# Kernel tuning notes

Hardware: AMD Instinct MI355X
Metric: run time of the kernel (lower is better)

The kernel has to match this reference:

```python
import jax, jax.numpy as jnp
import numpy as np

N_NODES = 50000
N_EDGES = 800000
HID = 64
N_GRAPHS = 64


def setup_inputs() -> dict:
    key = jax.random.key(0)
    ks = jax.random.split(key, 12)
    x = jax.random.normal(ks[0], (N_NODES, 1), dtype=jnp.float32)
    edge_index = jax.random.randint(ks[1], (2, N_EDGES), 0, N_NODES, dtype=jnp.int64)
    batch = jnp.sort(jax.random.randint(ks[2], (N_NODES,), 0, N_GRAPHS, dtype=jnp.int64))
    def glorot(k, shape):
        fan_in, fan_out = shape
        s = jnp.sqrt(2.0 / (fan_in + fan_out)).astype(jnp.float32)
        return jax.random.normal(k, shape, dtype=jnp.float32) * s
    return {
        "x": x, "edge_index": edge_index, "batch": batch,
        "W1l": glorot(ks[3], (1, HID)), "b1": jnp.zeros((HID,), jnp.float32), "W1r": glorot(ks[4], (1, HID)),
        "W2l": glorot(ks[5], (HID, HID)), "b2": jnp.zeros((HID,), jnp.float32), "W2r": glorot(ks[6], (HID, HID)),
        "W3l": glorot(ks[7], (HID, HID)), "b3": jnp.zeros((HID,), jnp.float32), "W3r": glorot(ks[8], (HID, HID)),
        "Wfc1": glorot(ks[9], (HID, HID // 2)), "bfc1": jnp.zeros((HID // 2,), jnp.float32),
        "Wfc2": glorot(ks[10], (HID // 2, 1)), "bfc2": jnp.zeros((1,), jnp.float32),
    }


def _sage_conv(x, src, dst, Wl, bl, Wr):
    # PyG SAGEConv (mean aggr): lin_l(mean_{j in N(i)} x_j) + lin_r(x_i)
    msgs = x[src]                                                   # [E, d] gather
    agg = jax.ops.segment_sum(msgs, dst, num_segments=N_NODES)      # [N, d] scatter-add
    cnt = jax.ops.segment_sum(jnp.ones((src.shape[0], 1), x.dtype), dst, num_segments=N_NODES)
    mean = agg / jnp.maximum(cnt, 1.0)                              # isolated nodes -> 0
    return mean @ Wl + bl + x @ Wr


def reference(x, edge_index, batch,
              W1l, b1, W1r, W2l, b2, W2r, W3l, b3, W3r,
              Wfc1, bfc1, Wfc2, bfc2):
    src, dst = edge_index[0], edge_index[1]
    layers = [(W1l, b1, W1r), (W2l, b2, W2r), (W3l, b3, W3r)]
    h = x
    for (Wl, bl, Wr) in layers:
        h_res = h
        h = jax.nn.relu(_sage_conv(h, src, dst, Wl, bl, Wr))
        # dropout is identity at inference; residual broadcasts [N,64]+[N,1] on layer 1
        h = h + h_res
    # global mean pool over graphs in the batch
    sums = jax.ops.segment_sum(h, batch, num_segments=N_GRAPHS)     # [G, d]
    cnts = jax.ops.segment_sum(jnp.ones((h.shape[0], 1), h.dtype), batch, num_segments=N_GRAPHS)
    pooled = sums / jnp.maximum(cnts, 1.0)
    out = jax.nn.relu(pooled @ Wfc1 + bfc1)
    out = out @ Wfc2 + bfc2                                          # [G, 1]
    return out
```

## Files before the change

kernel.cpp:

```cpp
#include <hip/hip_runtime.h>
#include <hip/hip_bf16.h>
#include <hip/hip_fp16.h>

#define HID 64
#define NGRAPHS 64
#define BUCKET 64
#define CAP 4096
#define EPB 2048
#define NSLOT 33

typedef _Float16 half8 __attribute__((ext_vector_type(8)));
typedef float floatx4 __attribute__((ext_vector_type(4)));

__global__ __launch_bounds__(256) void detect_init_kernel(const void* edge, const void* batch,
                                                          int* flags, int* bcursor,
                                                          float* psum,
                                                          const float* W2l, const float* W2r,
                                                          const float* W3l, const float* W3r,
                                                          __half* wl2h, __half* wr2h,
                                                          __half* wl3h, __half* wr3h,
                                                          int E2, int N, int G, int NB) {
    int t = threadIdx.x;
    for (int i = t; i < NB; i += 256) bcursor[i] = i * CAP;
    for (int i = t; i < G * HID; i += 256) psum[i] = 0.0f;
    for (int i = t; i < HID * HID; i += 256) {
        wl2h[i] = __float2half(W2l[i]);
        wr2h[i] = __float2half(W2r[i]);
        wl3h[i] = __float2half(W3l[i]);
        wr3h[i] = __float2half(W3r[i]);
    }
    if (t < 64) {
        int lane = t;
        int half_ = E2 / 2;
        int stride = half_ / 64; if (stride < 1) stride = 1;
        int j = lane * stride; if (j >= half_) j = half_ - 1;
        long long v = ((const long long*)edge)[j];
        bool ok = (v >= 0 && v < (long long)N);
        unsigned long long m = __ballot(ok);
        if (lane == 0) flags[0] = (m == ~0ULL) ? 1 : 0;
        int halfB = N / 2;
        int strideB = halfB / 64; if (strideB < 1) strideB = 1;
        int jb = lane * strideB; if (jb >= halfB) jb = halfB - 1;
        long long vb = ((const long long*)batch)[jb];
        bool okb = (vb >= 0 && vb < (long long)G);
        unsigned long long mb = __ballot(okb);
        if (lane == 0) flags[1] = (mb == ~0ULL) ? 1 : 0;
    }
}

__device__ __forceinline__ int idx_at(const void* p, int i, bool is64) {
    return is64 ? (int)((const long long*)p)[i] : ((const int*)p)[i];
}

__global__ __launch_bounds__(256) void bin_scatter_kernel(const void* edge, const int* __restrict__ flags,
                                                          int* __restrict__ bcursor,
                                                          unsigned int* __restrict__ entries,
                                                          int E, int NB) {
    extern __shared__ int lds[];
    int* hist = lds;
    int* base = lds + NB;
    int* ssrc = lds + 2 * NB;
    int* sdst = ssrc + EPB;
    for (int i = threadIdx.x; i < NB; i += 256) hist[i] = 0;
    __syncthreads();
    bool is64 = flags[0] != 0;
    int start = blockIdx.x * EPB;
    int end = start + EPB; if (end > E) end = E;
    int cnt = end - start;
    for (int k = threadIdx.x; k < cnt; k += 256) {
        int e = start + k;
        int srcv = idx_at(edge, e, is64);
        int d = idx_at(edge, E + e, is64);
        ssrc[k] = srcv;
        sdst[k] = d;
        atomicAdd(&hist[d >> 6], 1);
    }
    __syncthreads();
    for (int i = threadIdx.x; i < NB; i += 256) {
        int h = hist[i];
        base[i] = h ? atomicAdd(&bcursor[i], h) : 0;
    }
    __syncthreads();
    for (int i = threadIdx.x; i < NB; i += 256) hist[i] = 0;
    __syncthreads();
    for (int k = threadIdx.x; k < cnt; k += 256) {
        int d = sdst[k];
        int b = d >> 6;
        int lo = atomicAdd(&hist[b], 1);
        int p = base[b] + lo;
        if (p < (b + 1) * CAP)
            entries[p] = ((unsigned int)ssrc[k] << 6) | (unsigned int)(d & 63);
    }
}

__global__ __launch_bounds__(256) void csr_l1_kernel(const unsigned int* __restrict__ entries,
                                                     const int* __restrict__ bcursor,
                                                     const float* __restrict__ x,
                                                     const float* __restrict__ W1l,
                                                     const float* __restrict__ b1,
                                                     const float* __restrict__ W1r,
                                                     int* __restrict__ rowptr,
                                                     int* __restrict__ deg,
                                                     int* __restrict__ csr,
                                                     __half* __restrict__ h1h,
                                                     int N, int NB) {
    __shared__ int hist[BUCKET];
    __shared__ int lstart[BUCKET];
    __shared__ int lcur[BUCKET];
    __shared__ float accx[BUCKET];
    __shared__ float sx[BUCKET];
    int t = threadIdx.x;
    int b = blockIdx.x;
    int r0 = b * CAP;
    int cnt = bcursor[b] - r0; if (cnt > CAP) cnt = CAP;
    if (t < BUCKET) {
        hist[t] = 0; lcur[t] = 0; accx[t] = 0.0f;
        int node = b * BUCKET + t;
        sx[t] = (node < N) ? x[node] : 0.0f;
    }
    __syncthreads();
    for (int j = r0 + t; j < r0 + cnt; j += 256) {
        unsigned int en = entries[j];
        atomicAdd(&hist[en & 63u], 1);
        atomicAdd(&accx[en & 63u], x[en >> 6]);
    }
    __syncthreads();
    if (t < BUCKET) {
        int v = hist[t];
        int s = v;
#pragma unroll
        for (int off = 1; off < 64; off <<= 1) {
            int u = __shfl_up(s, off);
            if (t >= off) s += u;
        }
        lstart[t] = s - v;
        int node = b * BUCKET + t;
        if (node < N) {
            rowptr[node] = r0 + s - v;
            deg[node] = v;
        }
    }
    __syncthreads();
    for (int j = r0 + t; j < r0 + cnt; j += 256) {
        unsigned int en = entries[j];
        int dl = (int)(en & 63u);
        int p = atomicAdd(&lcur[dl], 1);
        csr[r0 + lstart[dl] + p] = (int)(en >> 6);
    }
    __syncthreads();
    int f = t & 63;
    int sub = t >> 6;
    float wlf = W1l[f], bf = b1[f], wrf = W1r[f];
    for (int it = 0; it < 16; ++it) {
        int nl = it * 4 + sub;
        int node = b * BUCKET + nl;
        if (node < N) {
            int d = hist[nl];
            float mv = (d > 0) ? accx[nl] / (float)d : 0.0f;
            float xv = sx[nl];
            float v = fmaf(mv, wlf, fmaf(xv, wrf, bf));
            v = v > 0.0f ? v : 0.0f;
            h1h[(size_t)node * HID + f] = __float2half(v + xv);
        }
    }
}

__global__ __launch_bounds__(256) void gather_mfma_kernel(const int* __restrict__ rowptr,
                                                          const int* __restrict__ deg,
                                                          const int* __restrict__ csr,
                                                          const __half* __restrict__ hph,
                                                          const __half* __restrict__ Wlh,
                                                          const float* __restrict__ bvec,
                                                          const __half* __restrict__ Wrh,
                                                          __half* __restrict__ houth,
                                                          float* __restrict__ psum,
                                                          const void* batch,
                                                          const int* __restrict__ flags,
                                                          int N) {
    __shared__ _Float16 smean[32][HID + 8];
    __shared__ float spool[NSLOT][HID];
    __shared__ int sb[32];
    int t = threadIdx.x;
    bool pool = (psum != nullptr);
    if (pool) {
        for (int i = t; i < NSLOT * HID; i += 256) ((float*)spool)[i] = 0.0f;
        if (t < 32) {
            int node = blockIdx.x * 32 + t;
            sb[t] = (node < N) ? idx_at(batch, node, flags[1] != 0) : -1;
        }
    }

    {
        int grp = t >> 3;
        int l = t & 7;
        int i = blockIdx.x * 32 + grp;
        if (i < N) {
            int r0 = rowptr[i];
            int d = deg[i];
            int r1 = r0 + d;
            float a[4][8];
#pragma unroll
            for (int w = 0; w < 4; ++w)
#pragma unroll
                for (int k = 0; k < 8; ++k) a[w][k] = 0.0f;
            int j = r0;
            for (; j + 8 <= r1; j += 8) {
                uint4 u[8];
#pragma unroll
                for (int m = 0; m < 8; ++m) {
                    int s = csr[j + m];
                    u[m] = *(const uint4*)(hph + (size_t)s * HID + l * 8);
                }
#pragma unroll
                for (int m = 0; m < 8; ++m) {
                    const __half2* p = (const __half2*)&u[m];
#pragma unroll
                    for (int q = 0; q < 4; ++q) {
                        float2 f2 = __half22float2(p[q]);
                        a[m & 3][2 * q]     += f2.x;
                        a[m & 3][2 * q + 1] += f2.y;
                    }
                }
            }
            for (; j + 4 <= r1; j += 4) {
                uint4 u[4];
#pragma unroll
                for (int m = 0; m < 4; ++m) {
                    int s = csr[j + m];
                    u[m] = *(const uint4*)(hph + (size_t)s * HID + l * 8);
                }
#pragma unroll
                for (int m = 0; m < 4; ++m) {
                    const __half2* p = (const __half2*)&u[m];
#pragma unroll
                    for (int q = 0; q < 4; ++q) {
                        float2 f2 = __half22float2(p[q]);
                        a[m][2 * q]     += f2.x;
                        a[m][2 * q + 1] += f2.y;
                    }
                }
            }
            for (; j < r1; ++j) {
                int s = csr[j];
                uint4 u0 = *(const uint4*)(hph + (size_t)s * HID + l * 8);
                const __half2* p = (const __half2*)&u0;
#pragma unroll
                for (int q = 0; q < 4; ++q) {
                    float2 f2 = __half22float2(p[q]);
                    a[0][2 * q]     += f2.x;
                    a[0][2 * q + 1] += f2.y;
                }
            }
            float inv = (d > 0) ? 1.0f / (float)d : 0.0f;
            __half2 o[4];
#pragma unroll
            for (int q = 0; q < 4; ++q) {
                float lo = ((a[0][2*q]   + a[1][2*q])   + (a[2][2*q]   + a[3][2*q]))   * inv;
                float hi = ((a[0][2*q+1] + a[1][2*q+1]) + (a[2][2*q+1] + a[3][2*q+1])) * inv;
                o[q] = __floats2half2_rn(lo, hi);
            }
            *(uint4*)&smean[grp][l * 8] = *(uint4*)o;
        }
    }
    __syncthreads();

    int wave = t >> 6;
    int lane = t & 63;
    int m = lane & 15;
    int quad = lane >> 4;
    int node0 = blockIdx.x * 32 + wave * 16;
    if (wave < 2 && node0 < N) {
        const _Float16* wlp = (const _Float16*)Wlh;
        const _Float16* wrp = (const _Float16*)Wrh;
        half8 bl[2][4], br[2][4];
#pragma unroll
        for (int kh = 0; kh < 2; ++kh)
#pragma unroll
            for (int nt = 0; nt < 4; ++nt) {
                half8 vl, vr;
#pragma unroll
                for (int j = 0; j < 8; ++j) {
                    int k = kh * 32 + quad * 8 + j;
                    vl[j] = wlp[k * HID + nt * 16 + m];
                    vr[j] = wrp[k * HID + nt * 16 + m];
                }
                bl[kh][nt] = vl;
                br[kh][nt] = vr;
            }
        int nlA = wave * 16 + m;
        half8 am0 = *(const half8*)&smean[nlA][quad * 8];
        half8 am1 = *(const half8*)&smean[nlA][32 + quad * 8];
        int nodeA = node0 + m; if (nodeA >= N) nodeA = N - 1;
        const _Float16* hrow = (const _Float16*)hph + (size_t)nodeA * HID;
        half8 ah0 = *(const half8*)(hrow + quad * 8);
        half8 ah1 = *(const half8*)(hrow + 32 + quad * 8);

#pragma unroll
        for (int nt = 0; nt < 4; ++nt) {
            float b = bvec[nt * 16 + m];
            floatx4 c = {b, b, b, b};
            c = __builtin_amdgcn_mfma_f32_16x16x32_f16(am0, bl[0][nt], c, 0, 0, 0);
            c = __builtin_amdgcn_mfma_f32_16x16x32_f16(am1, bl[1][nt], c, 0, 0, 0);
            c = __builtin_amdgcn_mfma_f32_16x16x32_f16(ah0, br[0][nt], c, 0, 0, 0);
            c = __builtin_amdgcn_mfma_f32_16x16x32_f16(ah1, br[1][nt], c, 0, 0, 0);
            int f = nt * 16 + m;
#pragma unroll
            for (int r = 0; r < 4; ++r) {
                int nodeR = node0 + quad * 4 + r;
                if (nodeR < N) {
                    float v = c[r];
                    v = v > 0.0f ? v : 0.0f;
                    v += __half2float(((const __half*)hph)[(size_t)nodeR * HID + f]);
                    if (!pool) {
                        houth[(size_t)nodeR * HID + f] = __float2half(v);
                    } else {
                        int bg = sb[wave * 16 + quad * 4 + r];
                        int slot = bg - sb[0];
                        if (slot < NSLOT) atomicAdd(&spool[slot][f], v);
                        else atomicAdd(&psum[bg * HID + f], v);
                    }
                }
            }
        }
    }

    if (pool) {
        __syncthreads();
        int gbase = sb[0];
        for (int i = t; i < NSLOT * HID; i += 256) {
            int s = i >> 6, f = i & 63;
            float v = spool[s][f];
            if (v != 0.0f) atomicAdd(&psum[(gbase + s) * HID + f], v);
        }
    }
}

__device__ __forceinline__ int lbound(const void* batch, int n, long long key, bool is64) {
    int lo = 0, hi = n;
    while (lo < hi) {
        int mid = (lo + hi) >> 1;
        long long v = is64 ? ((const long long*)batch)[mid] : (long long)((const int*)batch)[mid];
        if (v < key) lo = mid + 1; else hi = mid;
    }
    return lo;
}

__global__ __launch_bounds__(64) void fc_kernel(const float* __restrict__ psum,
                                                const void* batch,
                                                const int* __restrict__ flags,
                                                const float* __restrict__ Wfc1,
                                                const float* __restrict__ bfc1,
                                                const float* __restrict__ Wfc2,
                                                const float* __restrict__ bfc2,
                                                float* __restrict__ out, int N) {
    __shared__ int sb2[2];
    __shared__ float mean[HID];
    int g = blockIdx.x;
    int t = threadIdx.x;
    bool is64 = flags[1] != 0;
    if (t == 0) sb2[0] = lbound(batch, N, g, is64);
    if (t == 1) sb2[1] = lbound(batch, N, g + 1, is64);
    __syncthreads();
    float c = fmaxf((float)(sb2[1] - sb2[0]), 1.0f);
    mean[t] = psum[g * HID + t] / c;
    __syncthreads();
    float v = 0.0f;
    if (t < 32) {
        float acc = bfc1[t];
#pragma unroll
        for (int k = 0; k < HID; ++k) acc += mean[k] * Wfc1[k * 32 + t];
        float hcc = acc > 0.0f ? acc : 0.0f;
        v = hcc * Wfc2[t];
    }
#pragma unroll
    for (int off = 32; off >= 1; off >>= 1) v += __shfl_down(v, off);
    if (t == 0) out[g] = v + bfc2[0];
}

extern "C" void kernel_launch(void* const* d_in, const int* in_sizes, int n_in,
                              void* d_out, int out_size, void* d_ws, size_t ws_size,
                              hipStream_t stream) {
    const int N = in_sizes[0];
    const int E2 = in_sizes[1];
    const int E = E2 / 2;
    const int NB = (N + BUCKET - 1) / BUCKET;

    const float* x    = (const float*)d_in[0];
    const void*  edge = d_in[1];
    const void*  batch= d_in[2];
    const float* W1l  = (const float*)d_in[3];
    const float* b1   = (const float*)d_in[4];
    const float* W1r  = (const float*)d_in[5];
    const float* W2l  = (const float*)d_in[6];
    const float* b2   = (const float*)d_in[7];
    const float* W2r  = (const float*)d_in[8];
    const float* W3l  = (const float*)d_in[9];
    const float* b3   = (const float*)d_in[10];
    const float* W3r  = (const float*)d_in[11];
    const float* Wfc1 = (const float*)d_in[12];
    const float* bfc1 = (const float*)d_in[13];
    const float* Wfc2 = (const float*)d_in[14];
    const float* bfc2 = (const float*)d_in[15];
    float* out = (float*)d_out;

    char* ws = (char*)d_ws;
    size_t o = 0;
    auto alloc = [&](size_t bytes) { char* p = ws + o; o += (bytes + 255) & ~(size_t)255; return p; };
    int*   bcursor = (int*)alloc((size_t)NB * 4);
    float* psum    = (float*)alloc((size_t)NGRAPHS * HID * 4);
    unsigned int* entries = (unsigned int*)alloc((size_t)NB * CAP * 4);
    int*   csr     = (int*)alloc((size_t)NB * CAP * 4);
    int*   rowptr  = (int*)alloc((size_t)N * 4);
    int*   deg     = (int*)alloc((size_t)N * 4);
    __half* h1h    = (__half*)alloc((size_t)N * HID * 2);
    __half* h2h    = (__half*)alloc((size_t)N * HID * 2);
    __half* wl2h   = (__half*)alloc((size_t)HID * HID * 2);
    __half* wr2h   = (__half*)alloc((size_t)HID * HID * 2);
    __half* wl3h   = (__half*)alloc((size_t)HID * HID * 2);
    __half* wr3h   = (__half*)alloc((size_t)HID * HID * 2);
    int*   flags   = (int*)alloc(16);

    detect_init_kernel<<<1, 256, 0, stream>>>(edge, batch, flags, bcursor, psum,
                                              W2l, W2r, W3l, W3r, wl2h, wr2h, wl3h, wr3h,
                                              E2, N, NGRAPHS, NB);

    const int nblk = (E + EPB - 1) / EPB;
    const int scatter_lds = (2 * NB + 2 * EPB) * 4;
    bin_scatter_kernel<<<nblk, 256, scatter_lds, stream>>>(edge, flags, bcursor, entries, E, NB);

    csr_l1_kernel<<<NB, 256, 0, stream>>>(entries, bcursor, x, W1l, b1, W1r,
                                          rowptr, deg, csr, h1h, N, NB);

    const int fusedBlocks = (N + 31) / 32;

    gather_mfma_kernel<<<fusedBlocks, 256, 0, stream>>>(rowptr, deg, csr, h1h,
                                                        wl2h, b2, wr2h, h2h,
                                                        (float*)nullptr, nullptr, flags, N);

    gather_mfma_kernel<<<fusedBlocks, 256, 0, stream>>>(rowptr, deg, csr, h2h,
                                                        wl3h, b3, wr3h, (__half*)nullptr,
                                                        psum, batch, flags, N);

    fc_kernel<<<NGRAPHS, 64, 0, stream>>>(psum, batch, flags, Wfc1, bfc1, Wfc2, bfc2, out, N);
}
```

Baseline: 221.0 us.

## Gather neighbor features from an FP8 copy and spread weight conversion across blocks

Each layer now writes an extra FP8 copy of its node features, and the neighbor gather reads these 8-byte FP8 rows instead of 16-byte FP16 rows. The goal is to halve the bytes of the random-access gather, which dominates the two middle layers. The init kernel is also split over five blocks so the four weight conversions run in parallel. The cost is an extra FP8 store per layer and reduced precision in the mean aggregation, which may push outputs past tolerance. The 4-edge unrolled tail loop is also removed.

```diff
diff --git a/kernel.cpp b/kernel.cpp
--- a/kernel.cpp
+++ b/kernel.cpp
@@ -11,6 +11,12 @@
 
 typedef _Float16 half8 __attribute__((ext_vector_type(8)));
 typedef float floatx4 __attribute__((ext_vector_type(4)));
+typedef float floatx2 __attribute__((ext_vector_type(2)));
+
+__device__ __forceinline__ unsigned char enc_fp8(float v) {
+    int pk = __builtin_amdgcn_cvt_pk_fp8_f32(v, v, 0, false);
+    return (unsigned char)(pk & 0xff);
+}
 
 __global__ __launch_bounds__(256) void detect_init_kernel(const void* edge, const void* batch,
                                                           int* flags, int* bcursor,
@@ -21,30 +27,31 @@
                                                           __half* wl3h, __half* wr3h,
                                                           int E2, int N, int G, int NB) {
     int t = threadIdx.x;
-    for (int i = t; i < NB; i += 256) bcursor[i] = i * CAP;
-    for (int i = t; i < G * HID; i += 256) psum[i] = 0.0f;
-    for (int i = t; i < HID * HID; i += 256) {
-        wl2h[i] = __float2half(W2l[i]);
-        wr2h[i] = __float2half(W2r[i]);
-        wl3h[i] = __float2half(W3l[i]);
-        wr3h[i] = __float2half(W3r[i]);
-    }
-    if (t < 64) {
-        int lane = t;
-        int half_ = E2 / 2;
-        int stride = half_ / 64; if (stride < 1) stride = 1;
-        int j = lane * stride; if (j >= half_) j = half_ - 1;
-        long long v = ((const long long*)edge)[j];
-        bool ok = (v >= 0 && v < (long long)N);
-        unsigned long long m = __ballot(ok);
-        if (lane == 0) flags[0] = (m == ~0ULL) ? 1 : 0;
-        int halfB = N / 2;
-        int strideB = halfB / 64; if (strideB < 1) strideB = 1;
-        int jb = lane * strideB; if (jb >= halfB) jb = halfB - 1;
-        long long vb = ((const long long*)batch)[jb];
-        bool okb = (vb >= 0 && vb < (long long)G);
-        unsigned long long mb = __ballot(okb);
-        if (lane == 0) flags[1] = (mb == ~0ULL) ? 1 : 0;
+    int b = blockIdx.x;
+    if (b == 0) {
+        for (int i = t; i < NB; i += 256) bcursor[i] = i * CAP;
+        for (int i = t; i < G * HID; i += 256) psum[i] = 0.0f;
+        if (t < 64) {
+            int lane = t;
+            int half_ = E2 / 2;
+            int stride = half_ / 64; if (stride < 1) stride = 1;
+            int j = lane * stride; if (j >= half_) j = half_ - 1;
+            long long v = ((const long long*)edge)[j];
+            bool ok = (v >= 0 && v < (long long)N);
+            unsigned long long m = __ballot(ok);
+            if (lane == 0) flags[0] = (m == ~0ULL) ? 1 : 0;
+            int halfB = N / 2;
+            int strideB = halfB / 64; if (strideB < 1) strideB = 1;
+            int jb = lane * strideB; if (jb >= halfB) jb = halfB - 1;
+            long long vb = ((const long long*)batch)[jb];
+            bool okb = (vb >= 0 && vb < (long long)G);
+            unsigned long long mb = __ballot(okb);
+            if (lane == 0) flags[1] = (mb == ~0ULL) ? 1 : 0;
+        }
+    } else {
+        const float* src = (b == 1) ? W2l : (b == 2) ? W2r : (b == 3) ? W3l : W3r;
+        __half* dst = (b == 1) ? wl2h : (b == 2) ? wr2h : (b == 3) ? wl3h : wr3h;
+        for (int i = t; i < HID * HID; i += 256) dst[i] = __float2half(src[i]);
     }
 }
 
@@ -103,6 +110,7 @@
                                                      int* __restrict__ deg,
                                                      int* __restrict__ csr,
                                                      __half* __restrict__ h1h,
+                                                     unsigned char* __restrict__ h1q,
                                                      int N, int NB) {
     __shared__ int hist[BUCKET];
     __shared__ int lstart[BUCKET];
@@ -160,7 +168,9 @@
             float xv = sx[nl];
             float v = fmaf(mv, wlf, fmaf(xv, wrf, bf));
             v = v > 0.0f ? v : 0.0f;
-            h1h[(size_t)node * HID + f] = __float2half(v + xv);
+            float hv = v + xv;
+            h1h[(size_t)node * HID + f] = __float2half(hv);
+            h1q[(size_t)node * HID + f] = enc_fp8(hv);
         }
     }
 }
@@ -168,11 +178,13 @@
 __global__ __launch_bounds__(256) void gather_mfma_kernel(const int* __restrict__ rowptr,
                                                           const int* __restrict__ deg,
                                                           const int* __restrict__ csr,
+                                                          const unsigned char* __restrict__ hq,
                                                           const __half* __restrict__ hph,
                                                           const __half* __restrict__ Wlh,
                                                           const float* __restrict__ bvec,
                                                           const __half* __restrict__ Wrh,
                                                           __half* __restrict__ houth,
+                                                          unsigned char* __restrict__ houtq,
                                                           float* __restrict__ psum,
                                                           const void* batch,
                                                           const int* __restrict__ flags,
@@ -205,51 +217,36 @@
                 for (int k = 0; k < 8; ++k) a[w][k] = 0.0f;
             int j = r0;
             for (; j + 8 <= r1; j += 8) {
-                uint4 u[8];
+                uint2 u[8];
 #pragma unroll
                 for (int m = 0; m < 8; ++m) {
                     int s = csr[j + m];
-                    u[m] = *(const uint4*)(hph + (size_t)s * HID + l * 8);
+                    u[m] = *(const uint2*)(hq + (size_t)s * HID + l * 8);
                 }
 #pragma unroll
                 for (int m = 0; m < 8; ++m) {
-                    const __half2* p = (const __half2*)&u[m];
-#pragma unroll
-                    for (int q = 0; q < 4; ++q) {
-                        float2 f2 = __half22float2(p[q]);
-                        a[m & 3][2 * q]     += f2.x;
-                        a[m & 3][2 * q + 1] += f2.y;
-                    }
-                }
-            }
-            for (; j + 4 <= r1; j += 4) {
-                uint4 u[4];
-#pragma unroll
-                for (int m = 0; m < 4; ++m) {
-                    int s = csr[j + m];
-                    u[m] = *(const uint4*)(hph + (size_t)s * HID + l * 8);
-                }
-#pragma unroll
-                for (int m = 0; m < 4; ++m) {
-                    const __half2* p = (const __half2*)&u[m];
-#pragma unroll
-                    for (int q = 0; q < 4; ++q) {
-                        float2 f2 = __half22float2(p[q]);
-                        a[m][2 * q]     += f2.x;
-                        a[m][2 * q + 1] += f2.y;
-                    }
+                    floatx2 p0 = __builtin_amdgcn_cvt_pk_f32_fp8(u[m].x, false);
+                    floatx2 p1 = __builtin_amdgcn_cvt_pk_f32_fp8(u[m].x, true);
+                    floatx2 p2 = __builtin_amdgcn_cvt_pk_f32_fp8(u[m].y, false);
+                    floatx2 p3 = __builtin_amdgcn_cvt_pk_f32_fp8(u[m].y, true);
+                    int w = m & 3;
+                    a[w][0] += p0[0]; a[w][1] += p0[1];
+                    a[w][2] += p1[0]; a[w][3] += p1[1];
+                    a[w][4] += p2[0]; a[w][5] += p2[1];
+                    a[w][6] += p3[0]; a[w][7] += p3[1];
                 }
             }
             for (; j < r1; ++j) {
                 int s = csr[j];
-                uint4 u0 = *(const uint4*)(hph + (size_t)s * HID + l * 8);
-                const __half2* p = (const __half2*)&u0;
-#pragma unroll
-                for (int q = 0; q < 4; ++q) {
-                    float2 f2 = __half22float2(p[q]);
-                    a[0][2 * q]     += f2.x;
-                    a[0][2 * q + 1] += f2.y;
-                }
+                uint2 u0 = *(const uint2*)(hq + (size_t)s * HID + l * 8);
+                floatx2 p0 = __builtin_amdgcn_cvt_pk_f32_fp8(u0.x, false);
+                floatx2 p1 = __builtin_amdgcn_cvt_pk_f32_fp8(u0.x, true);
+                floatx2 p2 = __builtin_amdgcn_cvt_pk_f32_fp8(u0.y, false);
+                floatx2 p3 = __builtin_amdgcn_cvt_pk_f32_fp8(u0.y, true);
+                a[0][0] += p0[0]; a[0][1] += p0[1];
+                a[0][2] += p1[0]; a[0][3] += p1[1];
+                a[0][4] += p2[0]; a[0][5] += p2[1];
+                a[0][6] += p3[0]; a[0][7] += p3[1];
             }
             float inv = (d > 0) ? 1.0f / (float)d : 0.0f;
             __half2 o[4];
@@ -313,6 +310,7 @@
                     v += __half2float(((const __half*)hph)[(size_t)nodeR * HID + f]);
                     if (!pool) {
                         houth[(size_t)nodeR * HID + f] = __float2half(v);
+                        houtq[(size_t)nodeR * HID + f] = enc_fp8(v);
                     } else {
                         int bg = sb[wave * 16 + quad * 4 + r];
                         int slot = bg - sb[0];
@@ -414,13 +412,15 @@
     int*   deg     = (int*)alloc((size_t)N * 4);
     __half* h1h    = (__half*)alloc((size_t)N * HID * 2);
     __half* h2h    = (__half*)alloc((size_t)N * HID * 2);
+    unsigned char* h1q = (unsigned char*)alloc((size_t)N * HID);
+    unsigned char* h2q = (unsigned char*)alloc((size_t)N * HID);
     __half* wl2h   = (__half*)alloc((size_t)HID * HID * 2);
     __half* wr2h   = (__half*)alloc((size_t)HID * HID * 2);
     __half* wl3h   = (__half*)alloc((size_t)HID * HID * 2);
     __half* wr3h   = (__half*)alloc((size_t)HID * HID * 2);
     int*   flags   = (int*)alloc(16);
 
-    detect_init_kernel<<<1, 256, 0, stream>>>(edge, batch, flags, bcursor, psum,
+    detect_init_kernel<<<5, 256, 0, stream>>>(edge, batch, flags, bcursor, psum,
                                               W2l, W2r, W3l, W3r, wl2h, wr2h, wl3h, wr3h,
                                               E2, N, NGRAPHS, NB);
 
@@ -429,16 +429,17 @@
     bin_scatter_kernel<<<nblk, 256, scatter_lds, stream>>>(edge, flags, bcursor, entries, E, NB);
 
     csr_l1_kernel<<<NB, 256, 0, stream>>>(entries, bcursor, x, W1l, b1, W1r,
-                                          rowptr, deg, csr, h1h, N, NB);
+                                          rowptr, deg, csr, h1h, h1q, N, NB);
 
     const int fusedBlocks = (N + 31) / 32;
 
-    gather_mfma_kernel<<<fusedBlocks, 256, 0, stream>>>(rowptr, deg, csr, h1h,
-                                                        wl2h, b2, wr2h, h2h,
+    gather_mfma_kernel<<<fusedBlocks, 256, 0, stream>>>(rowptr, deg, csr, h1q, h1h,
+                                                        wl2h, b2, wr2h, h2h, h2q,
                                                         (float*)nullptr, nullptr, flags, N);
 
-    gather_mfma_kernel<<<fusedBlocks, 256, 0, stream>>>(rowptr, deg, csr, h2h,
+    gather_mfma_kernel<<<fusedBlocks, 256, 0, stream>>>(rowptr, deg, csr, h2q, h2h,
                                                         wl3h, b3, wr3h, (__half*)nullptr,
+                                                        (unsigned char*)nullptr,
                                                         psum, batch, flags, N);
 
     fc_kernel<<<NGRAPHS, 64, 0, stream>>>(psum, batch, flags, Wfc1, bfc1, Wfc2, bfc2, out, N);
```

New measurement: 209.2 us. -5.3%, faster.
